# Performance work log

Measured on AMD Instinct MI355X. Metric: run time of the kernel, lower is better.

## Reference

```python
import jax, jax.numpy as jnp
import numpy as np

B, F_IN, T_IN = 256, 3, 800
C, K, H, N_OUT = 128, 15, 150, 10

def hard_sigmoid(x):
    # Keras-style hard sigmoid used by LSTMHardSigmoid: clamp(0.2*x + 0.5, 0, 1)
    return jnp.clip(0.2 * x + 0.5, 0.0, 1.0)

def setup_inputs() -> dict:
    key = jax.random.key(0)
    ks = jax.random.split(key, 16)
    mk = lambda k, s, sc=0.05: (jax.random.normal(k, s, dtype=jnp.float32) * sc)
    return {
        "x": jax.random.normal(ks[0], (B, F_IN, T_IN), dtype=jnp.float32),
        "conv_w": mk(ks[1], (C, F_IN, K), 0.1),
        "conv_b": jnp.zeros((C,), jnp.float32),
        # PyTorch LSTM layout: [4H, in] with gate order i,f,g,o
        "w_ih_f": mk(ks[2], (4 * H, C)),
        "w_hh_f": mk(ks[3], (4 * H, H)),
        "b_ih_f": mk(ks[4], (4 * H,)),
        "b_hh_f": mk(ks[5], (4 * H,)),
        "w_ih_b": mk(ks[6], (4 * H, C)),
        "w_hh_b": mk(ks[7], (4 * H, H)),
        "b_ih_b": mk(ks[8], (4 * H,)),
        "b_hh_b": mk(ks[9], (4 * H,)),
        "lin1_w": mk(ks[10], (50, 2 * H)),
        "lin1_b": jnp.zeros((50,), jnp.float32),
        "lin2_w": mk(ks[11], (N_OUT, 50)),
        "lin2_b": jnp.zeros((N_OUT,), jnp.float32),
    }

def _lstm_dir(xseq, w_ih, w_hh, b_ih, b_hh, reverse):
    # xseq: [B, T, C] -> pre-activations [B, T, 4H]
    pre = jnp.einsum('btc,gc->btg', xseq, w_ih) + b_ih + b_hh
    pre_t = jnp.swapaxes(pre, 0, 1)  # [T, B, 4H]
    h0 = jnp.zeros((xseq.shape[0], H), pre.dtype)
    c0 = jnp.zeros((xseq.shape[0], H), pre.dtype)
    def step(carry, gt):
        h, c = carry
        g = gt + h @ w_hh.T
        i, f, gg, o = jnp.split(g, 4, axis=-1)
        c = hard_sigmoid(f) * c + hard_sigmoid(i) * jnp.tanh(gg)
        h = hard_sigmoid(o) * jnp.tanh(c)
        return (h, c), h
    _, hs = jax.lax.scan(step, (h0, c0), pre_t, reverse=reverse)
    return jnp.swapaxes(hs, 0, 1)  # [B, T, H]

def reference(x, conv_w, conv_b, w_ih_f, w_hh_f, b_ih_f, b_hh_f,
              w_ih_b, w_hh_b, b_ih_b, b_hh_b, lin1_w, lin1_b, lin2_w, lin2_b):
    # net1: Conv1d (VALID) + ReLU + (Dropout: identity at eval) + MaxPool1d(2)
    y = jax.lax.conv_general_dilated(
        x, conv_w, window_strides=(1,), padding='VALID',
        dimension_numbers=('NCH', 'OIH', 'NCH')) + conv_b[None, :, None]
    y = jax.nn.relu(y)                       # [B, 128, 786]
    L = y.shape[2] // 2
    y = y[:, :, :2 * L].reshape(y.shape[0], y.shape[1], L, 2).max(axis=-1)  # [B,128,393]
    xseq = jnp.transpose(y, (0, 2, 1))       # [B, 393, 128]
    # net2: bidirectional LSTM with hard-sigmoid gates
    h_fwd = _lstm_dir(xseq, w_ih_f, w_hh_f, b_ih_f, b_hh_f, reverse=False)
    h_bwd = _lstm_dir(xseq, w_ih_b, w_hh_b, b_ih_b, b_hh_b, reverse=True)
    bi = jnp.concatenate([h_fwd, h_bwd], axis=-1)  # [B, T, 300]
    # global max-pool over time (F.max_pool1d with kernel = full length)
    pooled = bi.max(axis=1)                  # [B, 300]
    # net3: Linear + ReLU + (Dropout identity) + Linear + Softmax(dim=1)
    z = jax.nn.relu(pooled @ lin1_w.T + lin1_b)
    logits = z @ lin2_w.T + lin2_b
    return jax.nn.softmax(logits, axis=1)
```

## Files before the change

kernel.cpp:

```cpp
#include <hip/hip_runtime.h>
#include <cstdio>

#define BATCH 256
#define TSEQ  393
#define CH    128
#define FIN   3
#define TIN   800
#define KK    15
#define HID   150
#define NPAD  640
#define KPAD  160
#define NB    16
#define PHASE 131
#define SLOTSTRIDE (16*10240)

typedef _Float16 half_t;
typedef __attribute__((ext_vector_type(8))) _Float16 h8v;
typedef __attribute__((ext_vector_type(4))) float f4v;

__device__ inline float hsig(float x){ return fminf(fmaxf(fmaf(0.2f, x, 0.5f), 0.f), 1.f); }
__device__ inline float tanh_(float x){
  float e = __expf(2.f*x);
  return fmaf(-2.f, __builtin_amdgcn_rcpf(e + 1.f), 1.f);
}

#define DPPF(v, ctrl) __int_as_float(__builtin_amdgcn_mov_dpp(__float_as_int(v), ctrl, 0xF, 0xF, true))
#define XPOSE_PAIR(va, vb, om, CTRL) { float t_ = om ? va : vb; t_ = DPPF(t_, CTRL); va = om ? t_ : va; vb = om ? vb : t_; }

__global__ void prep_wih(const float* __restrict__ wf, const float* __restrict__ wb,
                         half_t* __restrict__ out){
  int i = blockIdx.x*256 + threadIdx.x;
  if (i >= 2*NPAD*CH) return;
  int c = i & 127; int n = (i >> 7) % NPAD; int d = i / (NPAD*CH);
  const float* src = d ? wb : wf;
  float v = 0.f;
  if (n < 600){ int j = n >> 2, g = n & 3; v = src[(g*HID + j)*CH + c]; }
  out[i] = (half_t)v;
}
__global__ void prep_whh(const float* __restrict__ wf, const float* __restrict__ wb,
                         half_t* __restrict__ out){
  int i = blockIdx.x*256 + threadIdx.x;
  if (i >= 2*NPAD*KPAD) return;
  int kc = i % KPAD; int n = (i / KPAD) % NPAD; int d = i / (NPAD*KPAD);
  const float* src = d ? wb : wf;
  float v = 0.f;
  if (n < 600 && kc < HID){ int j = n >> 2, g = n & 3; v = src[(g*HID + j)*HID + kc]; }
  out[i] = (half_t)v;
}
__global__ void prep_bsum(const float* __restrict__ bihf, const float* __restrict__ bhhf,
                          const float* __restrict__ bihb, const float* __restrict__ bhhb,
                          float* __restrict__ out){
  int i = blockIdx.x*256 + threadIdx.x;
  if (i >= 2*NPAD) return;
  int n = i % NPAD; int d = i / NPAD;
  float v = 0.f;
  if (n < 600){ int j = n >> 2, g = n & 3; int r = g*HID + j;
    v = d ? (bihb[r] + bhhb[r]) : (bihf[r] + bhhf[r]); }
  out[i] = v;
}

#define CTT 32
__global__ __launch_bounds__(256) void conv_pool(const float* __restrict__ x,
                                                 const float* __restrict__ w,
                                                 const float* __restrict__ bias,
                                                 half_t* __restrict__ xseq){
  __shared__ float wl[CH*FIN*KK];
  __shared__ float xl[FIN][2*CTT + 14];
  int tid = threadIdx.x;
  int b = blockIdx.x, t0 = blockIdx.y*CTT;
  for (int i = tid; i < CH*FIN*KK; i += 256) wl[i] = w[i];
  int p0 = 2*t0;
  for (int i = tid; i < FIN*(2*CTT+14); i += 256){
    int f = i/(2*CTT+14), q = i%(2*CTT+14);
    int p = p0 + q;
    xl[f][q] = (p < TIN) ? x[((size_t)b*FIN + f)*TIN + p] : 0.f;
  }
  __syncthreads();
  int c = tid & 127, th = tid >> 7;
  float a0[16], a1[16];
  #pragma unroll
  for (int i=0;i<16;++i){ a0[i]=0.f; a1[i]=0.f; }
  #pragma unroll
  for (int f=0; f<FIN; ++f){
    float xv[46];
    #pragma unroll
    for (int q=0;q<46;++q) xv[q] = xl[f][th*32 + q];
    #pragma unroll
    for (int k=0;k<KK;++k){
      float ws = wl[c*FIN*KK + f*KK + k];
      #pragma unroll
      for (int i=0;i<16;++i){
        a0[i] = fmaf(xv[2*i+k],   ws, a0[i]);
        a1[i] = fmaf(xv[2*i+k+1], ws, a1[i]);
      }
    }
  }
  float bc = bias[c];
  #pragma unroll
  for (int i=0;i<16;++i){
    int t = t0 + th*16 + i;
    if (t < TSEQ){
      float v = fmaxf(fmaxf(a0[i], a1[i]) + bc, 0.f);
      xseq[((size_t)b*TSEQ + t)*CH + c] = (half_t)v;
    }
  }
}

__global__ __launch_bounds__(512) void proj(const half_t* __restrict__ xseq,
                                            const half_t* __restrict__ wih,
                                            const float* __restrict__ bsum,
                                            float* __restrict__ pre,
                                            int off){
  int bt4 = blockIdx.x;
  int s   = blockIdx.y;
  int d   = blockIdx.z;
  int sg  = s + off;
  int t   = d ? (TSEQ-1 - sg) : sg;
  int tid = threadIdx.x, wv = tid >> 6, ln = tid & 63;
  int m = ln & 15, kg = ln >> 4;

  h8v bfr[5][4]; float bs[5];
  #pragma unroll
  for (int i = 0; i < 5; ++i){
    int n = (wv*5 + i)*16 + m;
    #pragma unroll
    for (int ks = 0; ks < 4; ++ks)
      bfr[i][ks] = *(const h8v*)(wih + ((size_t)d*NPAD + n)*CH + ks*32 + kg*8);
    bs[i] = bsum[d*NPAD + n];
  }
  #pragma unroll
  for (int ms = 0; ms < 4; ++ms){
    int b = bt4*64 + ms*16 + m;
    h8v ax[4];
    #pragma unroll
    for (int ks = 0; ks < 4; ++ks)
      ax[ks] = *(const h8v*)(xseq + ((size_t)b*TSEQ + t)*CH + ks*32 + kg*8);
    #pragma unroll
    for (int i = 0; i < 5; ++i){
      f4v acc = {bs[i], bs[i], bs[i], bs[i]};
      #pragma unroll
      for (int ks = 0; ks < 4; ++ks)
        acc = __builtin_amdgcn_mfma_f32_16x16x32_f16(ax[ks], bfr[i][ks], acc, 0, 0, 0);
      int n = (wv*5 + i)*16 + m;
      *(f4v*)(pre + (((size_t)d*PHASE + s)*16 + (bt4*4 + ms))*10240 + n*16 + kg*4) = acc;
    }
  }
}

__global__ __launch_bounds__(512, 2) void recur(const float* __restrict__ pre,
                                                const half_t* __restrict__ whh,
                                                float* __restrict__ pooled,
                                                float* __restrict__ stateC,
                                                half_t* __restrict__ stateH,
                                                int first, int last){
  __shared__ __align__(16) half_t hbuf[2*NB*168];

  int tid = threadIdx.x, wv = tid >> 6, ln = tid & 63;
  int m = ln & 15, kg = ln >> 4;
  int bt = blockIdx.x, d = blockIdx.y;
  int b0 = bt*NB;
  int blk = d*16 + bt;
  bool o1 = (ln & 1), o2 = (ln & 2);

  h8v bhh[5][5];
  #pragma unroll
  for (int i = 0; i < 5; ++i){
    int n = (wv*5 + i)*16 + m;
    #pragma unroll
    for (int ks = 0; ks < 5; ++ks)
      bhh[i][ks] = *(const h8v*)(whh + ((size_t)d*NPAD + n)*KPAD + ks*32 + kg*8);
  }

  int jc[5], bc_;
  bc_ = kg*4 + (m&3);
  #pragma unroll
  for (int T = 0; T < 5; ++T) jc[T] = 20*wv + 4*T + (m>>2);

  float c_reg[5], hm_reg[5];
  if (first){
    for (int i = tid; i < NB*168; i += 512) hbuf[i] = (half_t)0.f;
    for (int i = tid; i < NB*168; i += 512) hbuf[NB*168 + i] = (half_t)0.f;
    #pragma unroll
    for (int T = 0; T < 5; ++T){ c_reg[T] = 0.f; hm_reg[T] = -1e30f; }
  } else {
    for (int i = tid; i < NB*168; i += 512) hbuf[i] = stateH[(size_t)blk*NB*168 + i];
    for (int i = tid; i < NB*168; i += 512) hbuf[NB*168 + i] = (half_t)0.f;
    const float* sc = stateC + ((size_t)blk*512 + tid)*10;
    #pragma unroll
    for (int T = 0; T < 5; ++T){ c_reg[T] = sc[T]; hm_reg[T] = sc[5+T]; }
  }
  __syncthreads();

  const float* psrc = pre + ((size_t)d*PHASE*16 + bt)*10240;
  int pofl = wv*1280 + m*16 + kg*4;

  f4v curp[5];
  #pragma unroll
  for (int T = 0; T < 5; ++T) curp[T] = *(const f4v*)(psrc + pofl + T*256);

  int p = 0;
  #pragma unroll 1
  for (int s = 0; s < PHASE; ++s){
    const float* nsrc = psrc + ((s+1 < PHASE) ? SLOTSTRIDE : 0);
    f4v nxt[5];
    #pragma unroll
    for (int T = 0; T < 5; ++T) nxt[T] = *(const f4v*)(nsrc + pofl + T*256);

    const half_t* hrd = hbuf + p*NB*168 + m*168;
    h8v ah[5];
    #pragma unroll
    for (int ks = 0; ks < 5; ++ks) ah[ks] = *(const h8v*)(hrd + ks*32 + kg*8);

    f4v acc[5];
    #pragma unroll
    for (int T = 0; T < 5; ++T){
      f4v a = {0.f, 0.f, 0.f, 0.f};
      #pragma unroll
      for (int ks = 0; ks < 5; ++ks)
        a = __builtin_amdgcn_mfma_f32_16x16x32_f16(ah[ks], bhh[T][ks], a, 0, 0, 0);
      acc[T] = a;
    }

    half_t* hwr = hbuf + (p^1)*NB*168 + bc_*168;
    #pragma unroll
    for (int T = 0; T < 5; ++T){
      float v0 = acc[T][0] + curp[T][0];
      float v1 = acc[T][1] + curp[T][1];
      float v2 = acc[T][2] + curp[T][2];
      float v3 = acc[T][3] + curp[T][3];
      XPOSE_PAIR(v0, v1, o1, 0xB1);
      XPOSE_PAIR(v2, v3, o1, 0xB1);
      XPOSE_PAIR(v0, v2, o2, 0x4E);
      XPOSE_PAIR(v1, v3, o2, 0x4E);
      float cn = hsig(v1)*c_reg[T] + hsig(v0)*tanh_(v2);
      float hn = hsig(v3)*tanh_(cn);
      c_reg[T] = cn;
      hm_reg[T] = fmaxf(hm_reg[T], hn);
      hwr[jc[T]] = (half_t)hn;
    }

    #pragma unroll
    for (int T = 0; T < 5; ++T) curp[T] = nxt[T];

    __syncthreads();
    p ^= 1;
    psrc += SLOTSTRIDE;
  }

  if (!last){
    for (int i = tid; i < NB*168; i += 512) stateH[(size_t)blk*NB*168 + i] = hbuf[p*NB*168 + i];
    float* sc = stateC + ((size_t)blk*512 + tid)*10;
    #pragma unroll
    for (int T = 0; T < 5; ++T){ sc[T] = c_reg[T]; sc[5+T] = hm_reg[T]; }
  } else {
    #pragma unroll
    for (int T = 0; T < 5; ++T){
      if (jc[T] < HID) pooled[(size_t)(b0 + bc_)*300 + d*HID + jc[T]] = hm_reg[T];
    }
  }
}

__global__ __launch_bounds__(256) void fc(const float* __restrict__ pooled,
                                          const float* __restrict__ w1, const float* __restrict__ b1,
                                          const float* __restrict__ w2, const float* __restrict__ b2,
                                          float* __restrict__ out){
  __shared__ float prow[300];
  __shared__ float ps[64][5];
  __shared__ float z[52];
  __shared__ float lg[12];
  int b = blockIdx.x, tid = threadIdx.x;
  for (int i = tid; i < 300; i += 256) prow[i] = pooled[(size_t)b*300 + i];
  __syncthreads();
  int j = tid & 63, seg = tid >> 6;
  float a = 0.f;
  if (j < 50){
    const float* wr = w1 + (size_t)j*300 + seg*75;
    const float* pr = prow + seg*75;
    #pragma unroll 5
    for (int k = 0; k < 75; ++k) a = fmaf(pr[k], wr[k], a);
  }
  ps[j][seg] = a;
  __syncthreads();
  if (tid < 50) z[tid] = fmaxf(ps[tid][0]+ps[tid][1]+ps[tid][2]+ps[tid][3] + b1[tid], 0.f);
  __syncthreads();
  if (tid < 10){
    float a2 = b2[tid];
    for (int k = 0; k < 50; ++k) a2 = fmaf(z[k], w2[tid*50 + k], a2);
    lg[tid] = a2;
  }
  __syncthreads();
  if (tid < 10){
    float mx = lg[0];
    #pragma unroll
    for (int k = 1; k < 10; ++k) mx = fmaxf(mx, lg[k]);
    float ssum = 0.f;
    #pragma unroll
    for (int k = 0; k < 10; ++k) ssum += __expf(lg[k] - mx);
    out[(size_t)b*10 + tid] = __expf(lg[tid] - mx) / ssum;
  }
}

extern "C" void kernel_launch(void* const* d_in, const int* in_sizes, int n_in,
                              void* d_out, int out_size, void* d_ws, size_t ws_size,
                              hipStream_t stream) {
  const float* x      = (const float*)d_in[0];
  const float* conv_w = (const float*)d_in[1];
  const float* conv_b = (const float*)d_in[2];
  const float* w_ih_f = (const float*)d_in[3];
  const float* w_hh_f = (const float*)d_in[4];
  const float* b_ih_f = (const float*)d_in[5];
  const float* b_hh_f = (const float*)d_in[6];
  const float* w_ih_b = (const float*)d_in[7];
  const float* w_hh_b = (const float*)d_in[8];
  const float* b_ih_b = (const float*)d_in[9];
  const float* b_hh_b = (const float*)d_in[10];
  const float* l1w = (const float*)d_in[11];
  const float* l1b = (const float*)d_in[12];
  const float* l2w = (const float*)d_in[13];
  const float* l2b = (const float*)d_in[14];
  float* out = (float*)d_out;

  char* ws = (char*)d_ws;
  size_t off = 0;
  auto alloc = [&](size_t bytes){ size_t o = off; off += (bytes + 255) & ~(size_t)255; return o; };
  size_t xseq_o = alloc((size_t)BATCH*TSEQ*CH*2);
  size_t pre_o  = alloc((size_t)2*PHASE*16*10240*4);
  size_t wih_o  = alloc((size_t)2*NPAD*CH*2);
  size_t whh_o  = alloc((size_t)2*NPAD*KPAD*2);
  size_t bs_o   = alloc((size_t)2*NPAD*4);
  size_t pool_o = alloc((size_t)BATCH*300*4);
  size_t stc_o  = alloc((size_t)32*512*10*4);
  size_t sth_o  = alloc((size_t)32*NB*168*2);
  if (off > ws_size){
    fprintf(stderr, "[cnnblstm] WS TOO SMALL: need %zu have %zu\n", off, ws_size);
    return;
  }
  half_t* xseq_p = (half_t*)(ws + xseq_o);
  float*  pre_p  = (float*)(ws + pre_o);
  half_t* wih_p  = (half_t*)(ws + wih_o);
  half_t* whh_p  = (half_t*)(ws + whh_o);
  float*  bs_p   = (float*)(ws + bs_o);
  float*  pool_p = (float*)(ws + pool_o);
  float*  stc_p  = (float*)(ws + stc_o);
  half_t* sth_p  = (half_t*)(ws + sth_o);

  prep_wih <<<(2*NPAD*CH + 255)/256, 256, 0, stream>>>(w_ih_f, w_ih_b, wih_p);
  prep_whh <<<(2*NPAD*KPAD + 255)/256, 256, 0, stream>>>(w_hh_f, w_hh_b, whh_p);
  prep_bsum<<<(2*NPAD + 255)/256, 256, 0, stream>>>(b_ih_f, b_hh_f, b_ih_b, b_hh_b, bs_p);
  conv_pool<<<dim3(BATCH, (TSEQ + CTT - 1)/CTT), 256, 0, stream>>>(x, conv_w, conv_b, xseq_p);

  for (int q = 0; q < 3; ++q){
    proj <<<dim3(4, PHASE, 2), 512, 0, stream>>>(xseq_p, wih_p, bs_p, pre_p, q*PHASE);
    recur<<<dim3(16, 2), 512, 0, stream>>>(pre_p, whh_p, pool_p, stc_p, sth_p, q==0, q==2);
  }

  fc<<<BATCH, 256, 0, stream>>>(pool_p, l1w, l1b, l2w, l2b, out);
}
```

Measured before the change: 726.6 us.

## Store LSTM pre-activations in fp16 and split the sequence into two phases

The input-projection buffer is now stored as fp16 instead of fp32. This halves its size, so the sequence can be processed in two chunks (197 and 196 steps) instead of three, which removes one proj/recur launch pair and one state save/restore. The recurrence loop swaps __syncthreads for an explicit lgkmcnt wait plus s_barrier with a sched_barrier, and pins the weight registers with an empty asm. The cost is reduced precision in the pre-activations added to the gates, and a longer recurrent kernel per launch.

```diff
diff --git a/kernel.cpp b/kernel.cpp
--- a/kernel.cpp
+++ b/kernel.cpp
@@ -11,11 +11,13 @@
 #define NPAD  640
 #define KPAD  160
 #define NB    16
-#define PHASE 131
+#define HALF_A 197
+#define HALF_B 196
 #define SLOTSTRIDE (16*10240)
 
 typedef _Float16 half_t;
 typedef __attribute__((ext_vector_type(8))) _Float16 h8v;
+typedef __attribute__((ext_vector_type(4))) _Float16 h4v;
 typedef __attribute__((ext_vector_type(4))) float f4v;
 
 __device__ inline float hsig(float x){ return fminf(fmaxf(fmaf(0.2f, x, 0.5f), 0.f), 1.f); }
@@ -109,7 +111,7 @@
 __global__ __launch_bounds__(512) void proj(const half_t* __restrict__ xseq,
                                             const half_t* __restrict__ wih,
                                             const float* __restrict__ bsum,
-                                            float* __restrict__ pre,
+                                            half_t* __restrict__ pre,
                                             int off){
   int bt4 = blockIdx.x;
   int s   = blockIdx.y;
@@ -142,17 +144,18 @@
       for (int ks = 0; ks < 4; ++ks)
         acc = __builtin_amdgcn_mfma_f32_16x16x32_f16(ax[ks], bfr[i][ks], acc, 0, 0, 0);
       int n = (wv*5 + i)*16 + m;
-      *(f4v*)(pre + (((size_t)d*PHASE + s)*16 + (bt4*4 + ms))*10240 + n*16 + kg*4) = acc;
-    }
-  }
-}
-
-__global__ __launch_bounds__(512, 2) void recur(const float* __restrict__ pre,
+      h4v hv = {(half_t)acc[0], (half_t)acc[1], (half_t)acc[2], (half_t)acc[3]};
+      *(h4v*)(pre + (((size_t)d*HALF_A + s)*16 + (bt4*4 + ms))*10240 + n*16 + kg*4) = hv;
+    }
+  }
+}
+
+__global__ __launch_bounds__(512, 2) void recur(const half_t* __restrict__ pre,
                                                 const half_t* __restrict__ whh,
                                                 float* __restrict__ pooled,
                                                 float* __restrict__ stateC,
                                                 half_t* __restrict__ stateH,
-                                                int first, int last){
+                                                int first, int last, int nsteps){
   __shared__ __align__(16) half_t hbuf[2*NB*168];
 
   int tid = threadIdx.x, wv = tid >> 6, ln = tid & 63;
@@ -170,6 +173,11 @@
     for (int ks = 0; ks < 5; ++ks)
       bhh[i][ks] = *(const h8v*)(whh + ((size_t)d*NPAD + n)*KPAD + ks*32 + kg*8);
   }
+  #pragma unroll
+  for (int i = 0; i < 5; ++i)
+    #pragma unroll
+    for (int ks = 0; ks < 5; ++ks)
+      asm volatile("" : "+v"(bhh[i][ks]));
 
   int jc[5], bc_;
   bc_ = kg*4 + (m&3);
@@ -191,20 +199,20 @@
   }
   __syncthreads();
 
-  const float* psrc = pre + ((size_t)d*PHASE*16 + bt)*10240;
+  const half_t* psrc = pre + ((size_t)d*HALF_A*16 + bt)*10240;
   int pofl = wv*1280 + m*16 + kg*4;
 
-  f4v curp[5];
-  #pragma unroll
-  for (int T = 0; T < 5; ++T) curp[T] = *(const f4v*)(psrc + pofl + T*256);
+  h4v curp[5];
+  #pragma unroll
+  for (int T = 0; T < 5; ++T) curp[T] = *(const h4v*)(psrc + pofl + T*256);
 
   int p = 0;
   #pragma unroll 1
-  for (int s = 0; s < PHASE; ++s){
-    const float* nsrc = psrc + ((s+1 < PHASE) ? SLOTSTRIDE : 0);
-    f4v nxt[5];
-    #pragma unroll
-    for (int T = 0; T < 5; ++T) nxt[T] = *(const f4v*)(nsrc + pofl + T*256);
+  for (int s = 0; s < nsteps; ++s){
+    const half_t* nsrc = psrc + ((s+1 < nsteps) ? SLOTSTRIDE : 0);
+    h4v nxt[5];
+    #pragma unroll
+    for (int T = 0; T < 5; ++T) nxt[T] = *(const h4v*)(nsrc + pofl + T*256);
 
     const half_t* hrd = hbuf + p*NB*168 + m*168;
     h8v ah[5];
@@ -224,10 +232,10 @@
     half_t* hwr = hbuf + (p^1)*NB*168 + bc_*168;
     #pragma unroll
     for (int T = 0; T < 5; ++T){
-      float v0 = acc[T][0] + curp[T][0];
-      float v1 = acc[T][1] + curp[T][1];
-      float v2 = acc[T][2] + curp[T][2];
-      float v3 = acc[T][3] + curp[T][3];
+      float v0 = acc[T][0] + (float)curp[T][0];
+      float v1 = acc[T][1] + (float)curp[T][1];
+      float v2 = acc[T][2] + (float)curp[T][2];
+      float v3 = acc[T][3] + (float)curp[T][3];
       XPOSE_PAIR(v0, v1, o1, 0xB1);
       XPOSE_PAIR(v2, v3, o1, 0xB1);
       XPOSE_PAIR(v0, v2, o2, 0x4E);
@@ -242,7 +250,9 @@
     #pragma unroll
     for (int T = 0; T < 5; ++T) curp[T] = nxt[T];
 
-    __syncthreads();
+    asm volatile("s_waitcnt lgkmcnt(0)" ::: "memory");
+    __builtin_amdgcn_s_barrier();
+    __builtin_amdgcn_sched_barrier(0);
     p ^= 1;
     psrc += SLOTSTRIDE;
   }
@@ -324,7 +334,7 @@
   size_t off = 0;
   auto alloc = [&](size_t bytes){ size_t o = off; off += (bytes + 255) & ~(size_t)255; return o; };
   size_t xseq_o = alloc((size_t)BATCH*TSEQ*CH*2);
-  size_t pre_o  = alloc((size_t)2*PHASE*16*10240*4);
+  size_t pre_o  = alloc((size_t)2*HALF_A*16*10240*2);
   size_t wih_o  = alloc((size_t)2*NPAD*CH*2);
   size_t whh_o  = alloc((size_t)2*NPAD*KPAD*2);
   size_t bs_o   = alloc((size_t)2*NPAD*4);
@@ -336,7 +346,7 @@
     return;
   }
   half_t* xseq_p = (half_t*)(ws + xseq_o);
-  float*  pre_p  = (float*)(ws + pre_o);
+  half_t* pre_p  = (half_t*)(ws + pre_o);
   half_t* wih_p  = (half_t*)(ws + wih_o);
   half_t* whh_p  = (half_t*)(ws + whh_o);
   float*  bs_p   = (float*)(ws + bs_o);
@@ -349,10 +359,10 @@
   prep_bsum<<<(2*NPAD + 255)/256, 256, 0, stream>>>(b_ih_f, b_hh_f, b_ih_b, b_hh_b, bs_p);
   conv_pool<<<dim3(BATCH, (TSEQ + CTT - 1)/CTT), 256, 0, stream>>>(x, conv_w, conv_b, xseq_p);
 
-  for (int q = 0; q < 3; ++q){
-    proj <<<dim3(4, PHASE, 2), 512, 0, stream>>>(xseq_p, wih_p, bs_p, pre_p, q*PHASE);
-    recur<<<dim3(16, 2), 512, 0, stream>>>(pre_p, whh_p, pool_p, stc_p, sth_p, q==0, q==2);
-  }
+  proj <<<dim3(4, HALF_A, 2), 512, 0, stream>>>(xseq_p, wih_p, bs_p, pre_p, 0);
+  recur<<<dim3(16, 2), 512, 0, stream>>>(pre_p, whh_p, pool_p, stc_p, sth_p, 1, 0, HALF_A);
+  proj <<<dim3(4, HALF_B, 2), 512, 0, stream>>>(xseq_p, wih_p, bs_p, pre_p, HALF_A);
+  recur<<<dim3(16, 2), 512, 0, stream>>>(pre_p, whh_p, pool_p, stc_p, sth_p, 0, 1, HALF_B);
 
   fc<<<BATCH, 256, 0, stream>>>(pool_p, l1w, l1b, l2w, l2b, out);
 }
```

Measured after the change: 666.7 us. 8.2% less time.
